# Optimization experiments

Measured on AMD Instinct MI355X. Metric: run time of the kernel, lower is better.

The kernel has to match this reference:

```python
import jax, jax.numpy as jnp
import numpy as np

BS, H, C = 32, 64, 64   # batch, spatial (square), channels == dim
S = 1                   # block size
DIM = 64                # codebook vector dim (per spatial cell)
K = 512                 # num_embeddings


def setup_inputs() -> dict:
    key = jax.random.key(0)
    k1, k2 = jax.random.split(key)
    x = jax.random.normal(k1, (BS, H, H, C), dtype=jnp.float32)
    # matches torch: randn(...).normal_(0, 0.02)
    embed = jax.random.normal(k2, (S, S, DIM, K), dtype=jnp.float32) * 0.02
    return {"x": x, "embed": embed}


def reference(x, embed):
    # Eval-mode forward of Quantize (EMA buffer updates only happen in training
    # and do not change the returned values).
    s, _, dim, k = embed.shape
    bs, hH, _, C = x.shape
    rH = hH // s
    # [bs, rH, rH, s, s, C] : group spatial into s x s blocks
    xr = jnp.transpose(x.reshape(bs, rH, s, rH, s, C), (0, 1, 3, 2, 4, 5))
    flat = xr.reshape(-1, s * s * dim)                    # [N, s*s*dim]
    ef = embed.reshape(-1, k)                             # [s*s*dim, K]
    # squared-distance matrix: ||f||^2 - 2 f.e + ||e||^2  -> [N, K]
    dist = ((flat * flat).sum(1, keepdims=True)
            - 2.0 * (flat @ ef)
            + (ef * ef).sum(0, keepdims=True))
    embed_ind = jnp.argmin(dist, axis=1)                  # == (-dist).max(1) indices
    embed_ind = embed_ind.reshape(bs, rH, rH)
    # gather codes: embed.permute(3,0,1,2)[ind] -> [bs, rH, rH, s, s, dim]
    codebook = jnp.transpose(embed, (3, 0, 1, 2))
    quantize = codebook[embed_ind]
    # perplexity exactly as in the source (mean over ALL one-hot entries -> scalar)
    p = jnp.mean(jax.nn.one_hot(embed_ind.reshape(-1), k, dtype=jnp.float32))
    perplexity = jnp.exp(-jnp.sum(p * jnp.log(p + 1e-10)))
    diff = jnp.mean((jax.lax.stop_gradient(quantize) - xr) ** 2)
    # straight-through estimator
    q_st = xr + jax.lax.stop_gradient(quantize - xr)
    out = jnp.swapaxes(q_st, 2, 3).reshape(bs, hH, hH, C)
    return (out, diff, embed_ind, perplexity)
```

## Files before the change

### kernel.cpp

```cpp
#include <hip/hip_runtime.h>
#include <math.h>

#define NROW  131072
#define DIMC  64
#define KCODE 512
#define BM    64
#define KC    128

__global__ void e2_kernel(const float* __restrict__ e, float* __restrict__ e2,
                          double* __restrict__ dacc) {
  int k = blockIdx.x * 256 + threadIdx.x;
  if (k == 0) *dacc = 0.0;
  if (k < KCODE) {
    float s = 0.f;
    for (int d = 0; d < DIMC; ++d) {
      float v = e[d * KCODE + k];
      s = __fadd_rn(s, __fmul_rn(v, v));
    }
    e2[k] = s;
  }
}

__global__ void __launch_bounds__(256)
quant_kernel(const float* __restrict__ x, const float* __restrict__ e,
             const float* __restrict__ e2, float* __restrict__ out,
             float* __restrict__ oidx, double* __restrict__ dacc) {
  __shared__ float xsT[DIMC][BM + 4];
  __shared__ float es[DIMC][KC];
  __shared__ float e2s[KC];
  __shared__ float ss[BM];
  __shared__ int   ridx[BM];

  const int t = threadIdx.x;
  const long row0 = (long)blockIdx.x * BM;
  const float* xblk = x + row0 * DIMC;

  for (int w = 0; w < 4; ++w) {
    int f = t + w * 256;
    int row = f >> 4;
    int c0 = (f & 15) * 4;
    float4 v = *(const float4*)(xblk + f * 4);
    xsT[c0 + 0][row] = v.x;
    xsT[c0 + 1][row] = v.y;
    xsT[c0 + 2][row] = v.z;
    xsT[c0 + 3][row] = v.w;
  }
  __syncthreads();

  if (t < BM) {
    float s = 0.f;
    for (int d = 0; d < DIMC; ++d) {
      float v = xsT[d][t];
      s = __fadd_rn(s, __fmul_rn(v, v));
    }
    ss[t] = s;
  }

  const int tc = t & 15;
  const int tr = t >> 4;
  float minv[4];
  int   mini[4];
  for (int r = 0; r < 4; ++r) { minv[r] = INFINITY; mini[r] = 0; }

  for (int chunk = 0; chunk < 4; ++chunk) {
    __syncthreads();
    for (int w = 0; w < 8; ++w) {
      int f = t + w * 256;
      int d = f >> 5;
      int cv = (f & 31) * 4;
      float4 v = *(const float4*)(e + d * KCODE + chunk * KC + cv);
      *(float4*)&es[d][cv] = v;
    }
    if (t < KC / 4)
      *(float4*)&e2s[t * 4] = *(const float4*)(e2 + chunk * KC + t * 4);
    __syncthreads();

    float acc[4][8];
    for (int r = 0; r < 4; ++r)
      for (int j = 0; j < 8; ++j) acc[r][j] = 0.f;

    for (int d = 0; d < DIMC; ++d) {
      float a[4], b[8];
      *(float4*)&a[0] = *(const float4*)&xsT[d][tr * 4];
      *(float4*)&b[0] = *(const float4*)&es[d][tc * 8];
      *(float4*)&b[4] = *(const float4*)&es[d][tc * 8 + 4];
      for (int r = 0; r < 4; ++r)
        for (int j = 0; j < 8; ++j)
          acc[r][j] = fmaf(a[r], b[j], acc[r][j]);
    }

    for (int r = 0; r < 4; ++r) {
      float sr = ss[tr * 4 + r];
      for (int j = 0; j < 8; ++j) {
        int col = chunk * KC + tc * 8 + j;
        float dist = __fadd_rn(__fsub_rn(sr, __fmul_rn(2.0f, acc[r][j])), e2s[tc * 8 + j]);
        if (dist < minv[r]) { minv[r] = dist; mini[r] = col; }
      }
    }
  }

  for (int off = 1; off < 16; off <<= 1) {
    for (int r = 0; r < 4; ++r) {
      float ov = __shfl_xor(minv[r], off, 16);
      int   oi = __shfl_xor(mini[r], off, 16);
      if (ov < minv[r] || (ov == minv[r] && oi < mini[r])) {
        minv[r] = ov; mini[r] = oi;
      }
    }
  }
  if (tc == 0)
    for (int r = 0; r < 4; ++r) ridx[tr * 4 + r] = mini[r];
  __syncthreads();

  if (t < BM) oidx[row0 + t] = (float)ridx[t];

  double dsum = 0.0;
  for (int i = 0; i < 16; ++i) {
    int l = i * 256 + t;
    int row = l >> 6;
    int c = l & 63;
    int idx = ridx[row];
    float xv = xsT[c][row];
    float q = e[c * KCODE + idx];
    out[row0 * DIMC + l] = __fadd_rn(xv, __fsub_rn(q, xv));
    float dq = __fsub_rn(q, xv);
    dsum += (double)__fmul_rn(dq, dq);
  }
  for (int off = 32; off > 0; off >>= 1)
    dsum += __shfl_down(dsum, off, 64);
  if ((t & 63) == 0) atomicAdd(dacc, dsum);
}

__global__ void fin_kernel(const double* __restrict__ dacc,
                           float* __restrict__ diff_out,
                           float* __restrict__ perp_out) {
  double s = *dacc;
  *diff_out = (float)(s / 8388608.0);
  float p = 1.0f / 512.0f;
  float lp = logf(p + 1e-10f);
  *perp_out = expf(-(p * lp));
}

extern "C" void kernel_launch(void* const* d_in, const int* in_sizes, int n_in,
                              void* d_out, int out_size, void* d_ws, size_t ws_size,
                              hipStream_t stream) {
  const float* x = (const float*)d_in[0];
  const float* e = (const float*)d_in[1];
  float* out  = (float*)d_out;
  float* diff = out + 8388608;
  float* oidx = out + 8388609;
  float* perp = out + 8388609 + 131072;

  float*  e2   = (float*)d_ws;
  double* dacc = (double*)((char*)d_ws + 2048);

  e2_kernel<<<2, 256, 0, stream>>>(e, e2, dacc);
  quant_kernel<<<NROW / BM, 256, 0, stream>>>(x, e, e2, out, oidx, dacc);
  fin_kernel<<<1, 1, 0, stream>>>(dacc, diff, perp);
}
```

Before: 239.0 us.

## Restructure quantizer to per-wave rows with lane-per-code, drop shared-memory tiling

Replaces the block-level shared-memory GEMM tiling with a wave-per-16-rows scheme. Each lane owns one code column per tile and reads x directly from global memory, with the x loads uniform across the wave so they act as broadcasts. Row norms move to a separate ss_kernel, and a transposed codebook eT is built so the final gather is coalesced. This removes LDS staging and barriers but relies on cache hits for repeated global x and e loads, keeps only a 16-row register tile per wave, and adds a kernel launch.

```diff
diff --git a/kernel.cpp b/kernel.cpp
--- a/kernel.cpp
+++ b/kernel.cpp
@@ -4,11 +4,14 @@
 #define NROW  131072
 #define DIMC  64
 #define KCODE 512
-#define BM    64
-#define KC    128
+#define RPW   16
+#define NTILE 8
+#define NBLK  (NROW / (4 * RPW))
 
-__global__ void e2_kernel(const float* __restrict__ e, float* __restrict__ e2,
-                          double* __restrict__ dacc) {
+typedef float f32x4 __attribute__((ext_vector_type(4)));
+
+__global__ void prep_kernel(const float* __restrict__ e, float* __restrict__ e2,
+                            float* __restrict__ eT, double* __restrict__ dacc) {
   int k = blockIdx.x * 256 + threadIdx.x;
   if (k == 0) *dacc = 0.0;
   if (k < KCODE) {
@@ -16,119 +19,104 @@
     for (int d = 0; d < DIMC; ++d) {
       float v = e[d * KCODE + k];
       s = __fadd_rn(s, __fmul_rn(v, v));
+      eT[k * DIMC + d] = v;
     }
     e2[k] = s;
   }
 }
 
+__global__ void ss_kernel(const float* __restrict__ x, float* __restrict__ ss) {
+  int row = blockIdx.x * 256 + threadIdx.x;
+  const float* xr = x + (long)row * DIMC;
+  float s = 0.f;
+#pragma unroll
+  for (int d0 = 0; d0 < DIMC; d0 += 4) {
+    f32x4 v = *(const f32x4*)(xr + d0);
+    s = __fadd_rn(s, __fmul_rn(v[0], v[0]));
+    s = __fadd_rn(s, __fmul_rn(v[1], v[1]));
+    s = __fadd_rn(s, __fmul_rn(v[2], v[2]));
+    s = __fadd_rn(s, __fmul_rn(v[3], v[3]));
+  }
+  ss[row] = s;
+}
+
 __global__ void __launch_bounds__(256)
 quant_kernel(const float* __restrict__ x, const float* __restrict__ e,
-             const float* __restrict__ e2, float* __restrict__ out,
+             const float* __restrict__ e2, const float* __restrict__ eT,
+             const float* __restrict__ ss, float* __restrict__ out,
              float* __restrict__ oidx, double* __restrict__ dacc) {
-  __shared__ float xsT[DIMC][BM + 4];
-  __shared__ float es[DIMC][KC];
-  __shared__ float e2s[KC];
-  __shared__ float ss[BM];
-  __shared__ int   ridx[BM];
+  const int lane = threadIdx.x & 63;
+  const int wid  = blockIdx.x * 4 + (threadIdx.x >> 6);
+  const long r0  = (long)wid * RPW;
 
-  const int t = threadIdx.x;
-  const long row0 = (long)blockIdx.x * BM;
-  const float* xblk = x + row0 * DIMC;
+  float ssr[RPW];
+#pragma unroll
+  for (int r = 0; r < RPW; ++r) ssr[r] = ss[r0 + r];
 
-  for (int w = 0; w < 4; ++w) {
-    int f = t + w * 256;
-    int row = f >> 4;
-    int c0 = (f & 15) * 4;
-    float4 v = *(const float4*)(xblk + f * 4);
-    xsT[c0 + 0][row] = v.x;
-    xsT[c0 + 1][row] = v.y;
-    xsT[c0 + 2][row] = v.z;
-    xsT[c0 + 3][row] = v.w;
-  }
-  __syncthreads();
+  float minv[RPW];
+  int   mini[RPW];
+#pragma unroll
+  for (int r = 0; r < RPW; ++r) { minv[r] = INFINITY; mini[r] = 0; }
 
-  if (t < BM) {
-    float s = 0.f;
-    for (int d = 0; d < DIMC; ++d) {
-      float v = xsT[d][t];
-      s = __fadd_rn(s, __fmul_rn(v, v));
-    }
-    ss[t] = s;
-  }
+  for (int T = 0; T < NTILE; ++T) {
+    const int col = T * 64 + lane;
+    const float e2v = e2[col];
+    const float* ecol = e + col;
 
-  const int tc = t & 15;
-  const int tr = t >> 4;
-  float minv[4];
-  int   mini[4];
-  for (int r = 0; r < 4; ++r) { minv[r] = INFINITY; mini[r] = 0; }
+    float acc[RPW];
+#pragma unroll
+    for (int r = 0; r < RPW; ++r) acc[r] = 0.f;
 
-  for (int chunk = 0; chunk < 4; ++chunk) {
-    __syncthreads();
-    for (int w = 0; w < 8; ++w) {
-      int f = t + w * 256;
-      int d = f >> 5;
-      int cv = (f & 31) * 4;
-      float4 v = *(const float4*)(e + d * KCODE + chunk * KC + cv);
-      *(float4*)&es[d][cv] = v;
-    }
-    if (t < KC / 4)
-      *(float4*)&e2s[t * 4] = *(const float4*)(e2 + chunk * KC + t * 4);
-    __syncthreads();
-
-    float acc[4][8];
-    for (int r = 0; r < 4; ++r)
-      for (int j = 0; j < 8; ++j) acc[r][j] = 0.f;
-
-    for (int d = 0; d < DIMC; ++d) {
-      float a[4], b[8];
-      *(float4*)&a[0] = *(const float4*)&xsT[d][tr * 4];
-      *(float4*)&b[0] = *(const float4*)&es[d][tc * 8];
-      *(float4*)&b[4] = *(const float4*)&es[d][tc * 8 + 4];
-      for (int r = 0; r < 4; ++r)
-        for (int j = 0; j < 8; ++j)
-          acc[r][j] = fmaf(a[r], b[j], acc[r][j]);
+    for (int d0 = 0; d0 < DIMC; d0 += 4) {
+      float b0 = ecol[(d0 + 0) * KCODE];
+      float b1 = ecol[(d0 + 1) * KCODE];
+      float b2 = ecol[(d0 + 2) * KCODE];
+      float b3 = ecol[(d0 + 3) * KCODE];
+#pragma unroll
+      for (int r = 0; r < RPW; ++r) {
+        f32x4 av = *(const f32x4*)(x + (r0 + r) * DIMC + d0);
+        acc[r] = fmaf(av[0], b0, acc[r]);
+        acc[r] = fmaf(av[1], b1, acc[r]);
+        acc[r] = fmaf(av[2], b2, acc[r]);
+        acc[r] = fmaf(av[3], b3, acc[r]);
+      }
     }
 
-    for (int r = 0; r < 4; ++r) {
-      float sr = ss[tr * 4 + r];
-      for (int j = 0; j < 8; ++j) {
-        int col = chunk * KC + tc * 8 + j;
-        float dist = __fadd_rn(__fsub_rn(sr, __fmul_rn(2.0f, acc[r][j])), e2s[tc * 8 + j]);
-        if (dist < minv[r]) { minv[r] = dist; mini[r] = col; }
-      }
+#pragma unroll
+    for (int r = 0; r < RPW; ++r) {
+      float dist = __fadd_rn(__fsub_rn(ssr[r], __fmul_rn(2.0f, acc[r])), e2v);
+      if (dist < minv[r]) { minv[r] = dist; mini[r] = col; }
     }
   }
 
-  for (int off = 1; off < 16; off <<= 1) {
-    for (int r = 0; r < 4; ++r) {
-      float ov = __shfl_xor(minv[r], off, 16);
-      int   oi = __shfl_xor(mini[r], off, 16);
+#pragma unroll
+  for (int off = 1; off < 64; off <<= 1) {
+#pragma unroll
+    for (int r = 0; r < RPW; ++r) {
+      float ov = __shfl_xor(minv[r], off, 64);
+      int   oi = __shfl_xor(mini[r], off, 64);
       if (ov < minv[r] || (ov == minv[r] && oi < mini[r])) {
         minv[r] = ov; mini[r] = oi;
       }
     }
   }
-  if (tc == 0)
-    for (int r = 0; r < 4; ++r) ridx[tr * 4 + r] = mini[r];
-  __syncthreads();
-
-  if (t < BM) oidx[row0 + t] = (float)ridx[t];
 
   double dsum = 0.0;
-  for (int i = 0; i < 16; ++i) {
-    int l = i * 256 + t;
-    int row = l >> 6;
-    int c = l & 63;
-    int idx = ridx[row];
-    float xv = xsT[c][row];
-    float q = e[c * KCODE + idx];
-    out[row0 * DIMC + l] = __fadd_rn(xv, __fsub_rn(q, xv));
+#pragma unroll
+  for (int r = 0; r < RPW; ++r) {
+    const long row = r0 + r;
+    const int  idx = mini[r];
+    float xv = x[row * DIMC + lane];
+    float q  = eT[(long)idx * DIMC + lane];
+    out[row * DIMC + lane] = __fadd_rn(xv, __fsub_rn(q, xv));
     float dq = __fsub_rn(q, xv);
     dsum += (double)__fmul_rn(dq, dq);
+    if (lane == 0) oidx[row] = (float)idx;
   }
+#pragma unroll
   for (int off = 32; off > 0; off >>= 1)
     dsum += __shfl_down(dsum, off, 64);
-  if ((t & 63) == 0) atomicAdd(dacc, dsum);
+  if (lane == 0) atomicAdd(dacc, dsum);
 }
 
 __global__ void fin_kernel(const double* __restrict__ dacc,
@@ -153,8 +141,11 @@
 
   float*  e2   = (float*)d_ws;
   double* dacc = (double*)((char*)d_ws + 2048);
+  float*  eT   = (float*)((char*)d_ws + 4096);
+  float*  ss   = (float*)((char*)d_ws + 4096 + 131072);
 
-  e2_kernel<<<2, 256, 0, stream>>>(e, e2, dacc);
-  quant_kernel<<<NROW / BM, 256, 0, stream>>>(x, e, e2, out, oidx, dacc);
+  prep_kernel<<<2, 256, 0, stream>>>(e, e2, eT, dacc);
+  ss_kernel<<<NROW / 256, 256, 0, stream>>>(x, ss);
+  quant_kernel<<<NBLK, 256, 0, stream>>>(x, e, e2, eT, ss, out, oidx, dacc);
   fin_kernel<<<1, 1, 0, stream>>>(dacc, diff, perp);
 }
```

Result: slower. 663.0 us (+177.4%).
